# Kernel tuning notes

Measured on AMD Instinct MI355X. Metric: run time of the kernel, lower is better.

## Reference

```python
import jax, jax.numpy as jnp
import numpy as np

N = 100000   # nodes
E = 1600000  # edges (avg degree 16)
N_IN, N_HID, N_OUT = 64, 64, 16


def setup_inputs() -> dict:
    key = jax.random.key(0)
    k1, k2, k3, k4 = jax.random.split(key, 4)
    x = jax.random.normal(k1, (N, N_IN), dtype=jnp.float32)
    edge_index = jax.random.randint(k2, (2, E), 0, N, dtype=jnp.int64)
    # Glorot-style init like PyG GCNConv linear weights
    W1 = jax.random.normal(k3, (N_IN, N_HID), dtype=jnp.float32) * (1.0 / np.sqrt(N_IN))
    b1 = jnp.zeros((N_HID,), dtype=jnp.float32)
    W2 = jax.random.normal(k4, (N_HID, N_OUT), dtype=jnp.float32) * (1.0 / np.sqrt(N_HID))
    b2 = jnp.zeros((N_OUT,), dtype=jnp.float32)
    return {"x": x, "edge_index": edge_index, "W1": W1, "b1": b1, "W2": W2, "b2": b2}


def reference(x, edge_index, W1, b1, W2, b2):
    n = x.shape[0]
    # GCNConv default: add self-loops with weight 1, symmetric normalization
    loop = jnp.arange(n, dtype=edge_index.dtype)
    src = jnp.concatenate([edge_index[0], loop])  # [E+N]
    dst = jnp.concatenate([edge_index[1], loop])  # [E+N]
    w = jnp.ones(src.shape[0], dtype=x.dtype)
    deg = jax.ops.segment_sum(w, dst, num_segments=n)           # in-degree incl. self-loop
    dinv = jnp.where(deg > 0, jax.lax.rsqrt(deg), 0.0)
    norm = dinv[src] * w * dinv[dst]                            # [E+N] edge coefficients

    def gcn_conv(h, Wm, bm):
        h = h @ Wm                                              # [N, d_out] linear first (PyG order)
        msg = h[src] * norm[:, None]                            # gather + scale
        return jax.ops.segment_sum(msg, dst, num_segments=n) + bm  # scatter-add + bias

    h = jax.nn.relu(gcn_conv(x, W1, b1))
    # dropout is identity at inference (training=False)
    return jax.nn.log_softmax(gcn_conv(h, W2, b2), axis=1)
```

## Files before the change

### kernel.cpp

```cpp
#include <hip/hip_runtime.h>

constexpr int FIN = 64;
constexpr int FH  = 64;
constexpr int FO  = 16;


constexpr int BSH      = 7;
constexpr int BW       = 1 << BSH;
constexpr int NBUCK    = 1024;
constexpr int EPB      = 16384;

constexpr int XSTR     = 68;

__device__ inline unsigned short f2bf(float f) {
    unsigned u = __float_as_uint(f);
    return (unsigned short)((u + 0x7FFFu + ((u >> 16) & 1u)) >> 16);
}
__device__ inline float bf2f(unsigned short h) {
    return __uint_as_float((unsigned)h << 16);
}
__device__ inline float4 bf4_to_f4(ushort4 u) {
    float4 f;
    f.x = bf2f(u.x); f.y = bf2f(u.y); f.z = bf2f(u.z); f.w = bf2f(u.w);
    return f;
}

__launch_bounds__(256)
__global__ void hist_kernel(const int* __restrict__ ei, int E,
                            int* __restrict__ bcnt, int* __restrict__ gchist) {
    __shared__ int lh[NBUCK];
    int t = threadIdx.x;
    for (int i = t; i < NBUCK; i += 256) lh[i] = 0;
    __syncthreads();
    int base = blockIdx.x * EPB;
    int lim  = min(E, base + EPB);
    for (int e = base + t; e < lim; e += 256)
        atomicAdd(&lh[ei[E + e] >> BSH], 1);
    __syncthreads();
    int* gh = gchist + (size_t)blockIdx.x * NBUCK;
    for (int b = t; b < NBUCK; b += 256) {
        int c = lh[b];
        gh[b] = c;
        if (c > 0) atomicAdd(&bcnt[b], c);
    }
}

__launch_bounds__(1024)
__global__ void bucket_scan_kernel(const int* __restrict__ bcnt, int* __restrict__ bbase,
                                   const int* __restrict__ gchist, int* __restrict__ gbase,
                                   int NCH, int* __restrict__ offs, int N, int E) {
    __shared__ int s[NBUCK];
    int t = threadIdx.x;
    int v = bcnt[t];
    s[t] = v;
    __syncthreads();
    for (int d = 1; d < NBUCK; d <<= 1) {
        int u = (t >= d) ? s[t - d] : 0;
        __syncthreads();
        s[t] += u;
        __syncthreads();
    }
    int ex = s[t] - v;
    bbase[t] = ex;
    if (t == NBUCK - 1) {
        bbase[NBUCK] = s[t];
        offs[N] = E;
    }
    int run = ex;
    #pragma unroll 4
    for (int c = 0; c < NCH; ++c) {
        gbase[(size_t)c * NBUCK + t] = run;
        run += gchist[(size_t)c * NBUCK + t];
    }
}

__device__ inline void binning_body(const int* __restrict__ ei, int E, int chunk,
                                    const int* __restrict__ gbase,
                                    unsigned* __restrict__ ebuf, int* lh) {
    int t = threadIdx.x;
    const int* gb = gbase + (size_t)chunk * NBUCK;
    for (int i = t; i < NBUCK; i += 256) lh[i] = gb[i];
    __syncthreads();
    int base = chunk * EPB;
    int lim  = min(E, base + EPB);
    for (int e = base + t; e < lim; e += 256) {
        int d    = ei[E + e];
        int srcv = ei[e];
        int pos = atomicAdd(&lh[d >> BSH], 1);
        ebuf[pos] = (unsigned)srcv | ((unsigned)(d & (BW - 1)) << 17);
    }
}

__launch_bounds__(256)
__global__ void binning_kernel(const int* __restrict__ ei, int E,
                               const int* __restrict__ gbase, unsigned* __restrict__ ebuf) {
    __shared__ int lh[NBUCK];
    binning_body(ei, E, blockIdx.x, gbase, ebuf, lh);
}

__launch_bounds__(256, 4)
__global__ void gemm1_binning_kernel(const float* __restrict__ x, const float* __restrict__ W1,
                                     unsigned short* __restrict__ hsb,
                                     const int* __restrict__ ei, int E,
                                     const int* __restrict__ gbase, unsigned* __restrict__ ebuf,
                                     int N, int NBIN) {
    __shared__ float smem[FIN * FH + 64 * XSTR];
    int tid = threadIdx.x;
    if ((int)blockIdx.x < NBIN) {
        binning_body(ei, E, (int)blockIdx.x, gbase, ebuf, (int*)smem);
        return;
    }
    float* Ws = smem;
    float* Xs = smem + FIN * FH;
    int rowBase = ((int)blockIdx.x - NBIN) * 64;
    {
        const float4* W14 = (const float4*)W1;
        float4* Ws4 = (float4*)Ws;
        #pragma unroll
        for (int i = tid; i < 1024; i += 256) Ws4[i] = W14[i];
        const float4* x4 = (const float4*)x;
        #pragma unroll
        for (int i = tid; i < 1024; i += 256) {
            int row = i >> 4, kq = i & 15;
            int gr = min(rowBase + row, N - 1);
            *(float4*)&Xs[row * XSTR + kq * 4] = x4[(size_t)gr * 16 + kq];
        }
    }
    __syncthreads();
    int cg = tid & 15;
    int rg = tid >> 4;
    int r0 = rowBase + rg * 4;
    float4 acc0 = {0,0,0,0}, acc1 = {0,0,0,0}, acc2 = {0,0,0,0}, acc3 = {0,0,0,0};
    #pragma unroll 2
    for (int kc = 0; kc < 16; ++kc) {
        float4 xa0 = *(const float4*)&Xs[(rg * 4 + 0) * XSTR + kc * 4];
        float4 xa1 = *(const float4*)&Xs[(rg * 4 + 1) * XSTR + kc * 4];
        float4 xa2 = *(const float4*)&Xs[(rg * 4 + 2) * XSTR + kc * 4];
        float4 xa3 = *(const float4*)&Xs[(rg * 4 + 3) * XSTR + kc * 4];
        const float* xa0f = (const float*)&xa0;
        const float* xa1f = (const float*)&xa1;
        const float* xa2f = (const float*)&xa2;
        const float* xa3f = (const float*)&xa3;
        #pragma unroll
        for (int j = 0; j < 4; ++j) {
            float4 wv = *(const float4*)&Ws[(kc * 4 + j) * FH + cg * 4];
            float v0 = xa0f[j], v1 = xa1f[j], v2 = xa2f[j], v3 = xa3f[j];
            acc0.x = fmaf(v0, wv.x, acc0.x); acc0.y = fmaf(v0, wv.y, acc0.y);
            acc0.z = fmaf(v0, wv.z, acc0.z); acc0.w = fmaf(v0, wv.w, acc0.w);
            acc1.x = fmaf(v1, wv.x, acc1.x); acc1.y = fmaf(v1, wv.y, acc1.y);
            acc1.z = fmaf(v1, wv.z, acc1.z); acc1.w = fmaf(v1, wv.w, acc1.w);
            acc2.x = fmaf(v2, wv.x, acc2.x); acc2.y = fmaf(v2, wv.y, acc2.y);
            acc2.z = fmaf(v2, wv.z, acc2.z); acc2.w = fmaf(v2, wv.w, acc2.w);
            acc3.x = fmaf(v3, wv.x, acc3.x); acc3.y = fmaf(v3, wv.y, acc3.y);
            acc3.z = fmaf(v3, wv.z, acc3.z); acc3.w = fmaf(v3, wv.w, acc3.w);
        }
    }
    ushort4* hsb4 = (ushort4*)hsb;
    if (r0 + 0 < N) hsb4[(size_t)(r0 + 0) * 16 + cg] =
        make_ushort4(f2bf(acc0.x), f2bf(acc0.y), f2bf(acc0.z), f2bf(acc0.w));
    if (r0 + 1 < N) hsb4[(size_t)(r0 + 1) * 16 + cg] =
        make_ushort4(f2bf(acc1.x), f2bf(acc1.y), f2bf(acc1.z), f2bf(acc1.w));
    if (r0 + 2 < N) hsb4[(size_t)(r0 + 2) * 16 + cg] =
        make_ushort4(f2bf(acc2.x), f2bf(acc2.y), f2bf(acc2.z), f2bf(acc2.w));
    if (r0 + 3 < N) hsb4[(size_t)(r0 + 3) * 16 + cg] =
        make_ushort4(f2bf(acc3.x), f2bf(acc3.y), f2bf(acc3.z), f2bf(acc3.w));
}

__launch_bounds__(256)
__global__ void bucket_csr_kernel(const unsigned* __restrict__ ebuf,
                                  const int* __restrict__ bbase,
                                  int* __restrict__ csr, int* __restrict__ offs,
                                  float* __restrict__ dinv, int N) {
    __shared__ int cnt[BW], sc[BW], cur[BW];
    int t = threadIdx.x;
    int b = blockIdx.x;
    if (t < BW) cnt[t] = 0;
    __syncthreads();
    int beg = bbase[b], end = bbase[b + 1];
    for (int i = beg + t; i < end; i += 256)
        atomicAdd(&cnt[ebuf[i] >> 17], 1);
    __syncthreads();
    if (t < BW) sc[t] = cnt[t];
    __syncthreads();
    for (int d = 1; d < BW; d <<= 1) {
        int u = (t < BW && t >= d) ? sc[t - d] : 0;
        __syncthreads();
        if (t < BW) sc[t] += u;
        __syncthreads();
    }
    int nodeBase = b << BSH;
    if (t < BW) {
        int node = nodeBase + t;
        int ex = beg + sc[t] - cnt[t];
        cur[t] = ex;
        if (node < N) {
            offs[node] = ex;
            dinv[node] = rsqrtf((float)(cnt[t] + 1));
        }
    }
    __syncthreads();
    for (int i = beg + t; i < end; i += 256) {
        unsigned w = ebuf[i];
        int pos = atomicAdd(&cur[w >> 17], 1);
        csr[pos] = (int)(w & 0x1FFFF);
    }
}

__launch_bounds__(256)
__global__ void agg1_gemm2_kernel(const unsigned short* __restrict__ hsb,
                                  const int* __restrict__ csr,
                                  const int* __restrict__ offs, const float* __restrict__ dinv,
                                  const float* __restrict__ b1, const float* __restrict__ W2,
                                  unsigned short* __restrict__ hs2b, int N) {
    __shared__ float W2s[FH * FO];
    __shared__ float h1s[16][68];
    const ushort4* hs4 = (const ushort4*)hsb;
    int tid = threadIdx.x;
    for (int i = tid; i < FH * FO; i += 256) W2s[i] = W2[i];
    int g = tid >> 4, l = tid & 15;
    int n = blockIdx.x * 16 + g;
    if (n < N) {
        float di_n = dinv[n];
        float4 self = bf4_to_f4(hs4[(size_t)n * 16 + l]);
        float4 acc;
        acc.x = self.x * di_n; acc.y = self.y * di_n;
        acc.z = self.z * di_n; acc.w = self.w * di_n;
        int j = offs[n], end = offs[n + 1];
        for (; j + 7 < end; j += 8) {
            int s0 = csr[j],     s1 = csr[j + 1], s2 = csr[j + 2], s3 = csr[j + 3];
            int s4 = csr[j + 4], s5 = csr[j + 5], s6 = csr[j + 6], s7 = csr[j + 7];
            float d0 = dinv[s0], d1 = dinv[s1], d2 = dinv[s2], d3 = dinv[s3];
            float d4 = dinv[s4], d5 = dinv[s5], d6 = dinv[s6], d7 = dinv[s7];
            float4 a0 = bf4_to_f4(hs4[(size_t)s0 * 16 + l]);
            float4 a1 = bf4_to_f4(hs4[(size_t)s1 * 16 + l]);
            float4 a2 = bf4_to_f4(hs4[(size_t)s2 * 16 + l]);
            float4 a3 = bf4_to_f4(hs4[(size_t)s3 * 16 + l]);
            float4 a4 = bf4_to_f4(hs4[(size_t)s4 * 16 + l]);
            float4 a5 = bf4_to_f4(hs4[(size_t)s5 * 16 + l]);
            float4 a6 = bf4_to_f4(hs4[(size_t)s6 * 16 + l]);
            float4 a7 = bf4_to_f4(hs4[(size_t)s7 * 16 + l]);
            acc.x += (fmaf(a0.x, d0, a1.x * d1) + fmaf(a2.x, d2, a3.x * d3))
                   + (fmaf(a4.x, d4, a5.x * d5) + fmaf(a6.x, d6, a7.x * d7));
            acc.y += (fmaf(a0.y, d0, a1.y * d1) + fmaf(a2.y, d2, a3.y * d3))
                   + (fmaf(a4.y, d4, a5.y * d5) + fmaf(a6.y, d6, a7.y * d7));
            acc.z += (fmaf(a0.z, d0, a1.z * d1) + fmaf(a2.z, d2, a3.z * d3))
                   + (fmaf(a4.z, d4, a5.z * d5) + fmaf(a6.z, d6, a7.z * d7));
            acc.w += (fmaf(a0.w, d0, a1.w * d1) + fmaf(a2.w, d2, a3.w * d3))
                   + (fmaf(a4.w, d4, a5.w * d5) + fmaf(a6.w, d6, a7.w * d7));
        }
        for (; j + 1 < end; j += 2) {
            int s0 = csr[j], s1 = csr[j + 1];
            float d0 = dinv[s0], d1 = dinv[s1];
            float4 a0 = bf4_to_f4(hs4[(size_t)s0 * 16 + l]);
            float4 a1 = bf4_to_f4(hs4[(size_t)s1 * 16 + l]);
            acc.x += fmaf(a0.x, d0, a1.x * d1);
            acc.y += fmaf(a0.y, d0, a1.y * d1);
            acc.z += fmaf(a0.z, d0, a1.z * d1);
            acc.w += fmaf(a0.w, d0, a1.w * d1);
        }
        if (j < end) {
            int s0 = csr[j];
            float d0 = dinv[s0];
            float4 a0 = bf4_to_f4(hs4[(size_t)s0 * 16 + l]);
            acc.x = fmaf(a0.x, d0, acc.x); acc.y = fmaf(a0.y, d0, acc.y);
            acc.z = fmaf(a0.z, d0, acc.z); acc.w = fmaf(a0.w, d0, acc.w);
        }
        float4 bb = ((const float4*)b1)[l];
        float4 h;
        h.x = fmaxf(fmaf(di_n, acc.x, bb.x), 0.f);
        h.y = fmaxf(fmaf(di_n, acc.y, bb.y), 0.f);
        h.z = fmaxf(fmaf(di_n, acc.z, bb.z), 0.f);
        h.w = fmaxf(fmaf(di_n, acc.w, bb.w), 0.f);
        *((float4*)&h1s[g][l * 4]) = h;
    }
    __syncthreads();
    int r = tid >> 4, o = tid & 15;
    int n2 = blockIdx.x * 16 + r;
    if (n2 < N) {
        float acc = 0.f;
        #pragma unroll
        for (int jj = 0; jj < FH; ++jj)
            acc = fmaf(h1s[r][jj], W2s[jj * FO + o], acc);
        hs2b[(size_t)n2 * FO + o] = f2bf(acc * dinv[n2]);
    }
}

__launch_bounds__(256)
__global__ void agg2_softmax_kernel(const unsigned short* __restrict__ hs2b,
                                    const int* __restrict__ csr,
                                    const int* __restrict__ offs, const float* __restrict__ dinv,
                                    const float* __restrict__ b2, float* __restrict__ out, int N) {
    int tid = threadIdx.x;
    int g = tid >> 4, o = tid & 15;
    int n = blockIdx.x * 16 + g;
    float v = 0.f;
    if (n < N) {
        float acc = bf2f(hs2b[(size_t)n * 16 + o]);
        int j = offs[n], end = offs[n + 1];
        for (; j + 7 < end; j += 8) {
            int s0 = csr[j],     s1 = csr[j + 1], s2 = csr[j + 2], s3 = csr[j + 3];
            int s4 = csr[j + 4], s5 = csr[j + 5], s6 = csr[j + 6], s7 = csr[j + 7];
            float t0 = bf2f(hs2b[(size_t)s0 * 16 + o]) + bf2f(hs2b[(size_t)s1 * 16 + o]);
            float t1 = bf2f(hs2b[(size_t)s2 * 16 + o]) + bf2f(hs2b[(size_t)s3 * 16 + o]);
            float t2 = bf2f(hs2b[(size_t)s4 * 16 + o]) + bf2f(hs2b[(size_t)s5 * 16 + o]);
            float t3 = bf2f(hs2b[(size_t)s6 * 16 + o]) + bf2f(hs2b[(size_t)s7 * 16 + o]);
            acc += (t0 + t1) + (t2 + t3);
        }
        for (; j < end; ++j) acc += bf2f(hs2b[(size_t)csr[j] * 16 + o]);
        v = fmaf(dinv[n], acc, b2[o]);
    }
    float m = v;
    #pragma unroll
    for (int s = 8; s >= 1; s >>= 1) m = fmaxf(m, __shfl_xor(m, s, 64));
    float ex = __expf(v - m);
    float sum = ex;
    #pragma unroll
    for (int s = 8; s >= 1; s >>= 1) sum += __shfl_xor(sum, s, 64);
    if (n < N) out[(size_t)n * FO + o] = v - m - __logf(sum);
}

extern "C" void kernel_launch(void* const* d_in, const int* in_sizes, int n_in,
                              void* d_out, int out_size, void* d_ws, size_t ws_size,
                              hipStream_t stream) {
    const float* x  = (const float*)d_in[0];
    const int*   ei = (const int*)d_in[1];
    const float* W1 = (const float*)d_in[2];
    const float* b1 = (const float*)d_in[3];
    const float* W2 = (const float*)d_in[4];
    const float* b2 = (const float*)d_in[5];
    float* out = (float*)d_out;

    const int N = in_sizes[0] / FIN;
    const int E = in_sizes[1] / 2;
    const int NCH  = (E + EPB - 1) / EPB;
    const int NB4  = (N + BW - 1) / BW;
    const int G1T  = (N + 63) / 64;
    const int GA   = (N + 15) / 16;

    char* ws = (char*)d_ws;
    size_t off = 0;
    auto alloc = [&](size_t bytes) -> void* {
        off = (off + 255) & ~(size_t)255;
        void* p = ws + off;
        off += bytes;
        return p;
    };
    float*          dinv   = (float*)alloc((size_t)N * 4);
    unsigned short* hsb    = (unsigned short*)alloc((size_t)N * FH * 2);
    unsigned short* hs2b   = (unsigned short*)alloc((size_t)N * FO * 2);
    int*            offs   = (int*)alloc((size_t)(N + 1) * 4);
    int*            bcnt   = (int*)alloc(NBUCK * 4);
    int*            bbase  = (int*)alloc((NBUCK + 1) * 4);
    int*            gchist = (int*)alloc((size_t)NCH * NBUCK * 4);
    int*            gbase  = (int*)alloc((size_t)NCH * NBUCK * 4);
    unsigned* ebuf;
    int*      csr;
    bool ws_fits = (ws_size >= off + 512 + (size_t)E * 8);
    if (ws_fits) {
        ebuf = (unsigned*)alloc((size_t)E * 4);
        csr  = (int*)     alloc((size_t)E * 4);
    } else {
        ebuf = (unsigned*)x;
        csr  = (int*)x + E;
    }

    hipMemsetAsync(bcnt, 0, NBUCK * 4, stream);

    hist_kernel<<<NCH, 256, 0, stream>>>(ei, E, bcnt, gchist);
    bucket_scan_kernel<<<1, NBUCK, 0, stream>>>(bcnt, bbase, gchist, gbase, NCH,
                                                offs, N, E);
    if (ws_fits) {
        gemm1_binning_kernel<<<NCH + G1T, 256, 0, stream>>>(x, W1, hsb, ei, E,
                                                            gbase, ebuf, N, NCH);
    } else {
        gemm1_binning_kernel<<<G1T, 256, 0, stream>>>(x, W1, hsb, ei, E,
                                                      gbase, ebuf, N, 0);
        binning_kernel<<<NCH, 256, 0, stream>>>(ei, E, gbase, ebuf);
    }
    bucket_csr_kernel<<<NB4, 256, 0, stream>>>(ebuf, bbase, csr, offs, dinv, N);
    agg1_gemm2_kernel<<<GA, 256, 0, stream>>>(hsb, csr, offs, dinv, b1, W2, hs2b, N);
    agg2_softmax_kernel<<<GA, 256, 0, stream>>>(hs2b, csr, offs, dinv, b2, out, N);
}
```

Measured before the change: 217.5 us.

## Pre-scale layer-1 features by source dinv and batch edge loads

Per-node degree is now counted with global atomics in the histogram pass, and dinv is computed inside the GEMM1 blocks. Each transformed row is multiplied by its own dinv before the bf16 store, so the layer-1 aggregation no longer gathers dinv per edge. The edge loops in histogram, binning and CSR-build now load eight items per thread before issuing atomics, to raise memory-level parallelism. The chunk size drops to 4096 edges with 16-bit per-chunk histograms, which gives more blocks but more global atomics on deg and a longer serial scan over chunks.

```diff
diff --git a/kernel.cpp b/kernel.cpp
--- a/kernel.cpp
+++ b/kernel.cpp
@@ -8,7 +8,7 @@
 constexpr int BSH      = 7;
 constexpr int BW       = 1 << BSH;
 constexpr int NBUCK    = 1024;
-constexpr int EPB      = 16384;
+constexpr int EPB      = 4096;
 
 constexpr int XSTR     = 68;
 
@@ -27,27 +27,43 @@
 
 __launch_bounds__(256)
 __global__ void hist_kernel(const int* __restrict__ ei, int E,
-                            int* __restrict__ bcnt, int* __restrict__ gchist) {
+                            int* __restrict__ bcnt,
+                            unsigned short* __restrict__ gchist,
+                            int* __restrict__ deg) {
     __shared__ int lh[NBUCK];
     int t = threadIdx.x;
     for (int i = t; i < NBUCK; i += 256) lh[i] = 0;
     __syncthreads();
     int base = blockIdx.x * EPB;
     int lim  = min(E, base + EPB);
-    for (int e = base + t; e < lim; e += 256)
-        atomicAdd(&lh[ei[E + e] >> BSH], 1);
-    __syncthreads();
-    int* gh = gchist + (size_t)blockIdx.x * NBUCK;
+    for (int e0 = base + t; e0 < lim; e0 += 2048) {
+        int dd[8];
+        #pragma unroll
+        for (int q = 0; q < 8; ++q) {
+            int e = e0 + q * 256;
+            dd[q] = (e < lim) ? ei[E + e] : -1;
+        }
+        #pragma unroll
+        for (int q = 0; q < 8; ++q) {
+            if (dd[q] >= 0) {
+                atomicAdd(&lh[dd[q] >> BSH], 1);
+                atomicAdd(&deg[dd[q]], 1);
+            }
+        }
+    }
+    __syncthreads();
+    unsigned short* gh = gchist + (size_t)blockIdx.x * NBUCK;
     for (int b = t; b < NBUCK; b += 256) {
         int c = lh[b];
-        gh[b] = c;
+        gh[b] = (unsigned short)c;
         if (c > 0) atomicAdd(&bcnt[b], c);
     }
 }
 
 __launch_bounds__(1024)
 __global__ void bucket_scan_kernel(const int* __restrict__ bcnt, int* __restrict__ bbase,
-                                   const int* __restrict__ gchist, int* __restrict__ gbase,
+                                   const unsigned short* __restrict__ gchist,
+                                   int* __restrict__ gbase,
                                    int NCH, int* __restrict__ offs, int N, int E) {
     __shared__ int s[NBUCK];
     int t = threadIdx.x;
@@ -67,10 +83,10 @@
         offs[N] = E;
     }
     int run = ex;
-    #pragma unroll 4
+    #pragma unroll 16
     for (int c = 0; c < NCH; ++c) {
         gbase[(size_t)c * NBUCK + t] = run;
-        run += gchist[(size_t)c * NBUCK + t];
+        run += (int)gchist[(size_t)c * NBUCK + t];
     }
 }
 
@@ -83,11 +99,20 @@
     __syncthreads();
     int base = chunk * EPB;
     int lim  = min(E, base + EPB);
-    for (int e = base + t; e < lim; e += 256) {
-        int d    = ei[E + e];
-        int srcv = ei[e];
-        int pos = atomicAdd(&lh[d >> BSH], 1);
-        ebuf[pos] = (unsigned)srcv | ((unsigned)(d & (BW - 1)) << 17);
+    for (int e0 = base + t; e0 < lim; e0 += 2048) {
+        int dd[8], ss[8];
+        #pragma unroll
+        for (int q = 0; q < 8; ++q) {
+            int e = e0 + q * 256;
+            if (e < lim) { dd[q] = ei[E + e]; ss[q] = ei[e]; } else dd[q] = -1;
+        }
+        #pragma unroll
+        for (int q = 0; q < 8; ++q) {
+            if (dd[q] >= 0) {
+                int pos = atomicAdd(&lh[dd[q] >> BSH], 1);
+                ebuf[pos] = (unsigned)ss[q] | ((unsigned)(dd[q] & (BW - 1)) << 17);
+            }
+        }
     }
 }
 
@@ -103,15 +128,17 @@
                                      unsigned short* __restrict__ hsb,
                                      const int* __restrict__ ei, int E,
                                      const int* __restrict__ gbase, unsigned* __restrict__ ebuf,
+                                     const int* __restrict__ deg, float* __restrict__ dinv,
                                      int N, int NBIN) {
-    __shared__ float smem[FIN * FH + 64 * XSTR];
+    __shared__ float smem[FIN * FH + 64 * XSTR + 64];
     int tid = threadIdx.x;
     if ((int)blockIdx.x < NBIN) {
         binning_body(ei, E, (int)blockIdx.x, gbase, ebuf, (int*)smem);
         return;
     }
-    float* Ws = smem;
-    float* Xs = smem + FIN * FH;
+    float* Ws   = smem;
+    float* Xs   = smem + FIN * FH;
+    float* dvs  = smem + FIN * FH + 64 * XSTR;
     int rowBase = ((int)blockIdx.x - NBIN) * 64;
     {
         const float4* W14 = (const float4*)W1;
@@ -124,6 +151,12 @@
             int row = i >> 4, kq = i & 15;
             int gr = min(rowBase + row, N - 1);
             *(float4*)&Xs[row * XSTR + kq * 4] = x4[(size_t)gr * 16 + kq];
+        }
+        if (tid < 64) {
+            int gr = min(rowBase + tid, N - 1);
+            float dv = rsqrtf((float)(deg[gr] + 1));
+            dvs[tid] = dv;
+            if (rowBase + tid < N) dinv[rowBase + tid] = dv;
         }
     }
     __syncthreads();
@@ -155,30 +188,40 @@
             acc3.z = fmaf(v3, wv.z, acc3.z); acc3.w = fmaf(v3, wv.w, acc3.w);
         }
     }
+    float s0 = dvs[rg * 4 + 0], s1 = dvs[rg * 4 + 1];
+    float s2 = dvs[rg * 4 + 2], s3 = dvs[rg * 4 + 3];
     ushort4* hsb4 = (ushort4*)hsb;
     if (r0 + 0 < N) hsb4[(size_t)(r0 + 0) * 16 + cg] =
-        make_ushort4(f2bf(acc0.x), f2bf(acc0.y), f2bf(acc0.z), f2bf(acc0.w));
+        make_ushort4(f2bf(acc0.x*s0), f2bf(acc0.y*s0), f2bf(acc0.z*s0), f2bf(acc0.w*s0));
     if (r0 + 1 < N) hsb4[(size_t)(r0 + 1) * 16 + cg] =
-        make_ushort4(f2bf(acc1.x), f2bf(acc1.y), f2bf(acc1.z), f2bf(acc1.w));
+        make_ushort4(f2bf(acc1.x*s1), f2bf(acc1.y*s1), f2bf(acc1.z*s1), f2bf(acc1.w*s1));
     if (r0 + 2 < N) hsb4[(size_t)(r0 + 2) * 16 + cg] =
-        make_ushort4(f2bf(acc2.x), f2bf(acc2.y), f2bf(acc2.z), f2bf(acc2.w));
+        make_ushort4(f2bf(acc2.x*s2), f2bf(acc2.y*s2), f2bf(acc2.z*s2), f2bf(acc2.w*s2));
     if (r0 + 3 < N) hsb4[(size_t)(r0 + 3) * 16 + cg] =
-        make_ushort4(f2bf(acc3.x), f2bf(acc3.y), f2bf(acc3.z), f2bf(acc3.w));
+        make_ushort4(f2bf(acc3.x*s3), f2bf(acc3.y*s3), f2bf(acc3.z*s3), f2bf(acc3.w*s3));
 }
 
 __launch_bounds__(256)
 __global__ void bucket_csr_kernel(const unsigned* __restrict__ ebuf,
                                   const int* __restrict__ bbase,
-                                  int* __restrict__ csr, int* __restrict__ offs,
-                                  float* __restrict__ dinv, int N) {
+                                  int* __restrict__ csr, int* __restrict__ offs, int N) {
     __shared__ int cnt[BW], sc[BW], cur[BW];
     int t = threadIdx.x;
     int b = blockIdx.x;
     if (t < BW) cnt[t] = 0;
     __syncthreads();
     int beg = bbase[b], end = bbase[b + 1];
-    for (int i = beg + t; i < end; i += 256)
-        atomicAdd(&cnt[ebuf[i] >> 17], 1);
+    for (int i0 = beg + t; i0 < end; i0 += 2048) {
+        unsigned ww[8];
+        #pragma unroll
+        for (int q = 0; q < 8; ++q) {
+            int i = i0 + q * 256;
+            ww[q] = (i < end) ? ebuf[i] : 0xFFFFFFFFu;
+        }
+        #pragma unroll
+        for (int q = 0; q < 8; ++q)
+            if (ww[q] != 0xFFFFFFFFu) atomicAdd(&cnt[ww[q] >> 17], 1);
+    }
     __syncthreads();
     if (t < BW) sc[t] = cnt[t];
     __syncthreads();
@@ -193,16 +236,23 @@
         int node = nodeBase + t;
         int ex = beg + sc[t] - cnt[t];
         cur[t] = ex;
-        if (node < N) {
-            offs[node] = ex;
-            dinv[node] = rsqrtf((float)(cnt[t] + 1));
-        }
-    }
-    __syncthreads();
-    for (int i = beg + t; i < end; i += 256) {
-        unsigned w = ebuf[i];
-        int pos = atomicAdd(&cur[w >> 17], 1);
-        csr[pos] = (int)(w & 0x1FFFF);
+        if (node < N) offs[node] = ex;
+    }
+    __syncthreads();
+    for (int i0 = beg + t; i0 < end; i0 += 2048) {
+        unsigned ww[8];
+        #pragma unroll
+        for (int q = 0; q < 8; ++q) {
+            int i = i0 + q * 256;
+            ww[q] = (i < end) ? ebuf[i] : 0xFFFFFFFFu;
+        }
+        #pragma unroll
+        for (int q = 0; q < 8; ++q) {
+            if (ww[q] != 0xFFFFFFFFu) {
+                int pos = atomicAdd(&cur[ww[q] >> 17], 1);
+                csr[pos] = (int)(ww[q] & 0x1FFFF);
+            }
+        }
     }
 }
 
@@ -221,16 +271,11 @@
     int n = blockIdx.x * 16 + g;
     if (n < N) {
         float di_n = dinv[n];
-        float4 self = bf4_to_f4(hs4[(size_t)n * 16 + l]);
-        float4 acc;
-        acc.x = self.x * di_n; acc.y = self.y * di_n;
-        acc.z = self.z * di_n; acc.w = self.w * di_n;
+        float4 acc = bf4_to_f4(hs4[(size_t)n * 16 + l]);
         int j = offs[n], end = offs[n + 1];
         for (; j + 7 < end; j += 8) {
             int s0 = csr[j],     s1 = csr[j + 1], s2 = csr[j + 2], s3 = csr[j + 3];
             int s4 = csr[j + 4], s5 = csr[j + 5], s6 = csr[j + 6], s7 = csr[j + 7];
-            float d0 = dinv[s0], d1 = dinv[s1], d2 = dinv[s2], d3 = dinv[s3];
-            float d4 = dinv[s4], d5 = dinv[s5], d6 = dinv[s6], d7 = dinv[s7];
             float4 a0 = bf4_to_f4(hs4[(size_t)s0 * 16 + l]);
             float4 a1 = bf4_to_f4(hs4[(size_t)s1 * 16 + l]);
             float4 a2 = bf4_to_f4(hs4[(size_t)s2 * 16 + l]);
@@ -239,31 +284,21 @@
             float4 a5 = bf4_to_f4(hs4[(size_t)s5 * 16 + l]);
             float4 a6 = bf4_to_f4(hs4[(size_t)s6 * 16 + l]);
             float4 a7 = bf4_to_f4(hs4[(size_t)s7 * 16 + l]);
-            acc.x += (fmaf(a0.x, d0, a1.x * d1) + fmaf(a2.x, d2, a3.x * d3))
-                   + (fmaf(a4.x, d4, a5.x * d5) + fmaf(a6.x, d6, a7.x * d7));
-            acc.y += (fmaf(a0.y, d0, a1.y * d1) + fmaf(a2.y, d2, a3.y * d3))
-                   + (fmaf(a4.y, d4, a5.y * d5) + fmaf(a6.y, d6, a7.y * d7));
-            acc.z += (fmaf(a0.z, d0, a1.z * d1) + fmaf(a2.z, d2, a3.z * d3))
-                   + (fmaf(a4.z, d4, a5.z * d5) + fmaf(a6.z, d6, a7.z * d7));
-            acc.w += (fmaf(a0.w, d0, a1.w * d1) + fmaf(a2.w, d2, a3.w * d3))
-                   + (fmaf(a4.w, d4, a5.w * d5) + fmaf(a6.w, d6, a7.w * d7));
+            acc.x += ((a0.x + a1.x) + (a2.x + a3.x)) + ((a4.x + a5.x) + (a6.x + a7.x));
+            acc.y += ((a0.y + a1.y) + (a2.y + a3.y)) + ((a4.y + a5.y) + (a6.y + a7.y));
+            acc.z += ((a0.z + a1.z) + (a2.z + a3.z)) + ((a4.z + a5.z) + (a6.z + a7.z));
+            acc.w += ((a0.w + a1.w) + (a2.w + a3.w)) + ((a4.w + a5.w) + (a6.w + a7.w));
         }
         for (; j + 1 < end; j += 2) {
             int s0 = csr[j], s1 = csr[j + 1];
-            float d0 = dinv[s0], d1 = dinv[s1];
             float4 a0 = bf4_to_f4(hs4[(size_t)s0 * 16 + l]);
             float4 a1 = bf4_to_f4(hs4[(size_t)s1 * 16 + l]);
-            acc.x += fmaf(a0.x, d0, a1.x * d1);
-            acc.y += fmaf(a0.y, d0, a1.y * d1);
-            acc.z += fmaf(a0.z, d0, a1.z * d1);
-            acc.w += fmaf(a0.w, d0, a1.w * d1);
+            acc.x += a0.x + a1.x; acc.y += a0.y + a1.y;
+            acc.z += a0.z + a1.z; acc.w += a0.w + a1.w;
         }
         if (j < end) {
-            int s0 = csr[j];
-            float d0 = dinv[s0];
-            float4 a0 = bf4_to_f4(hs4[(size_t)s0 * 16 + l]);
-            acc.x = fmaf(a0.x, d0, acc.x); acc.y = fmaf(a0.y, d0, acc.y);
-            acc.z = fmaf(a0.z, d0, acc.z); acc.w = fmaf(a0.w, d0, acc.w);
+            float4 a0 = bf4_to_f4(hs4[(size_t)csr[j] * 16 + l]);
+            acc.x += a0.x; acc.y += a0.y; acc.z += a0.z; acc.w += a0.w;
         }
         float4 bb = ((const float4*)b1)[l];
         float4 h;
@@ -346,12 +381,13 @@
         return p;
     };
     float*          dinv   = (float*)alloc((size_t)N * 4);
+    int*            deg    = (int*)alloc((size_t)N * 4);
     unsigned short* hsb    = (unsigned short*)alloc((size_t)N * FH * 2);
     unsigned short* hs2b   = (unsigned short*)alloc((size_t)N * FO * 2);
     int*            offs   = (int*)alloc((size_t)(N + 1) * 4);
     int*            bcnt   = (int*)alloc(NBUCK * 4);
     int*            bbase  = (int*)alloc((NBUCK + 1) * 4);
-    int*            gchist = (int*)alloc((size_t)NCH * NBUCK * 4);
+    unsigned short* gchist = (unsigned short*)alloc((size_t)NCH * NBUCK * 2);
     int*            gbase  = (int*)alloc((size_t)NCH * NBUCK * 4);
     unsigned* ebuf;
     int*      csr;
@@ -365,19 +401,21 @@
     }
 
     hipMemsetAsync(bcnt, 0, NBUCK * 4, stream);
-
-    hist_kernel<<<NCH, 256, 0, stream>>>(ei, E, bcnt, gchist);
+    hipMemsetAsync(deg, 0, (size_t)N * 4, stream);
+
+    hist_kernel<<<NCH, 256, 0, stream>>>(ei, E, bcnt, gchist, deg);
     bucket_scan_kernel<<<1, NBUCK, 0, stream>>>(bcnt, bbase, gchist, gbase, NCH,
                                                 offs, N, E);
     if (ws_fits) {
         gemm1_binning_kernel<<<NCH + G1T, 256, 0, stream>>>(x, W1, hsb, ei, E,
-                                                            gbase, ebuf, N, NCH);
+                                                            gbase, ebuf, deg, dinv,
+                                                            N, NCH);
     } else {
         gemm1_binning_kernel<<<G1T, 256, 0, stream>>>(x, W1, hsb, ei, E,
-                                                      gbase, ebuf, N, 0);
+                                                      gbase, ebuf, deg, dinv, N, 0);
         binning_kernel<<<NCH, 256, 0, stream>>>(ei, E, gbase, ebuf);
     }
-    bucket_csr_kernel<<<NB4, 256, 0, stream>>>(ebuf, bbase, csr, offs, dinv, N);
+    bucket_csr_kernel<<<NB4, 256, 0, stream>>>(ebuf, bbase, csr, offs, N);
     agg1_gemm2_kernel<<<GA, 256, 0, stream>>>(hsb, csr, offs, dinv, b1, W2, hs2b, N);
     agg2_softmax_kernel<<<GA, 256, 0, stream>>>(hs2b, csr, offs, dinv, b2, out, N);
 }
```

Result: slower. 292.8 us (+34.6%).
